# Kernel tuning notes

Hardware: AMD Instinct MI355X
Metric: run time of the kernel (lower is better)

Reference implementation:

```python
import jax, jax.numpy as jnp
import numpy as np

HS = 512   # hidden_size
IN = 2048  # input_size
MB = 100   # memory_bank_size
T  = 4096  # nImg


def setup_inputs() -> dict:
    key = jax.random.key(0)
    ks = jax.random.split(key, 20)

    def w(k, i, o):
        return jax.random.normal(k, (i, o), jnp.float32) * (1.0 / np.sqrt(i))

    def b(k, o):
        return jax.random.normal(k, (o,), jnp.float32) * 0.01

    return {
        "hidden_out_a": jax.random.normal(ks[0], (T, IN), jnp.float32),
        "hidden_out_m": jax.random.normal(ks[1], (T, IN), jnp.float32),
        "W_ca": w(ks[2], HS + IN, HS),  "b_ca": b(ks[3], HS),    # hidden_to_content_a
        "W_cm": w(ks[4], HS + IN, HS),  "b_cm": b(ks[5], HS),    # hidden_to_content_m
        "W_wp": w(ks[6], 3 * HS, 3),    "b_wp": b(ks[7], 3),     # write_prob
        "W_wpa": w(ks[8], HS + IN, MB), "b_wpa": b(ks[9], MB),   # write_prob_a
        "W_wpm": w(ks[10], HS + IN, MB),"b_wpm": b(ks[11], MB),  # write_prob_m
        "W_rp": w(ks[12], 3 * HS, MB),  "b_rp": b(ks[13], MB),   # read_prob
        "W_rh": w(ks[14], 2 * HS, HS),  "b_rh": b(ks[15], HS),   # read_to_hidden
        "W_rha": w(ks[16], 2 * HS + IN, HS), "b_rha": b(ks[17], HS),  # read_to_hidden_a
        "W_rhm": w(ks[18], 2 * HS + IN, HS), "b_rhm": b(ks[19], HS),  # read_to_hidden_m
        "nImg": T,
    }


def reference(hidden_out_a, hidden_out_m,
              W_ca, b_ca, W_cm, b_cm,
              W_wp, b_wp, W_wpa, b_wpa, W_wpm, b_wpm,
              W_rp, b_rp, W_rh, b_rh,
              W_rha, b_rha, W_rhm, b_rhm,
              nImg):
    hs = W_rh.shape[1]
    mb = W_rp.shape[1]

    def step(carry, xs):
        mem, h, ha, hm = carry            # mem: [MB, HS]; h/ha/hm: [HS]
        xa, xm = xs                       # [IN] each
        xh = jnp.concatenate([ha, hm, h])               # [3*HS]
        ar = jax.nn.softmax(xh @ W_rp + b_rp)           # [MB]
        r = ar @ mem                                    # [HS] memory read
        h1 = jax.nn.relu(jnp.concatenate([r, h]) @ W_rh + b_rh)
        ha1 = jax.nn.relu(jnp.concatenate([xa, r, ha]) @ W_rha + b_rha)
        hm1 = jax.nn.relu(jnp.concatenate([xm, r, hm]) @ W_rhm + b_rhm)
        aw = jax.nn.softmax(xh @ W_wp + b_wp)           # [3] stream gate
        xha = jnp.concatenate([ha, xa])                 # [HS+IN]
        xhm = jnp.concatenate([hm, xm])
        c_a = jax.nn.relu(xha @ W_ca + b_ca)            # [HS]
        c_m = jax.nn.relu(xhm @ W_cm + b_cm)
        aw_a = jax.nn.softmax(xha @ W_wpa + b_wpa)      # [MB]
        aw_m = jax.nn.softmax(xhm @ W_wpm + b_wpm)
        mem = aw[0] * mem + aw[1] * aw_a[:, None] * c_a + aw[2] * aw_m[:, None] * c_m
        return (mem, h1, ha1, hm1), h1

    init = (jnp.zeros((mb, hs), hidden_out_a.dtype),
            jnp.zeros((hs,), hidden_out_a.dtype),
            jnp.zeros((hs,), hidden_out_a.dtype),
            jnp.zeros((hs,), hidden_out_a.dtype))
    _, hiddens = jax.lax.scan(step, init,
                              (hidden_out_a[:nImg], hidden_out_m[:nImg]))
    return hiddens  # [nImg, HS]
```

## Files before the change

### kernel.cpp

```cpp
#include <hip/hip_runtime.h>
#include <cstdint>
#include <cstddef>

#define HS 512

constexpr int TPB  = 512;
constexpr int GBLK = 64;
constexpr int OWNB = 24;
constexpr int WPAD = 516;

constexpr size_t OFF_TWrp  = 0;
constexpr size_t OFF_TWwp  = OFF_TWrp  + 100*1536;
constexpr size_t OFF_TWwpa = OFF_TWwp  + 3*1536;
constexpr size_t OFF_TWwpm = OFF_TWwpa + 100*512;
constexpr size_t OFF_TWca  = OFF_TWwpm + 100*512;
constexpr size_t OFF_TWcm  = OFF_TWca  + 512*512;
constexpr size_t OFF_TWh0  = OFF_TWcm  + 512*512;
constexpr size_t OFF_TWh1  = OFF_TWh0  + 512*512;
constexpr size_t OFF_TWh2  = OFF_TWh1  + 512*512;
constexpr size_t OFF_TWu0  = OFF_TWh2  + 512*512;
constexpr size_t OFF_TWu1  = OFF_TWu0  + 512*512;
constexpr size_t OFF_TWu2  = OFF_TWu1  + 512*512;
constexpr size_t OFF_PAca  = OFF_TWu2  + 512*512;
constexpr size_t OFF_PMcm  = OFF_PAca  + 4096*512;
constexpr size_t OFF_PArha = OFF_PMcm  + 4096*512;
constexpr size_t OFF_PMrhm = OFF_PArha + 4096*512;
constexpr size_t OFF_PAwpa = OFF_PMrhm + 4096*512;
constexpr size_t OFF_PMwpm = OFF_PAwpa + 4096*100;
constexpr size_t OFF_CARRY = OFF_PMwpm + 4096*100;
constexpr size_t OFF_BCAST = OFF_CARRY + 2*1536*2;

__device__ __forceinline__ unsigned long long ald(const unsigned long long* p) {
  return __hip_atomic_load(const_cast<unsigned long long*>(p),
                           __ATOMIC_RELAXED, __HIP_MEMORY_SCOPE_AGENT);
}
__device__ __forceinline__ void gstTag(unsigned long long* p, float v, unsigned tag) {
  unsigned long long u = ((unsigned long long)tag << 32) | (unsigned long long)__float_as_uint(v);
  __hip_atomic_store(p, u, __ATOMIC_RELAXED, __HIP_MEMORY_SCOPE_AGENT);
}
__device__ __forceinline__ float xrsum(float v) {
  #pragma unroll
  for (int o = 32; o; o >>= 1) v += __shfl_xor(v, o, 64);
  return v;
}
__device__ __forceinline__ float rsum16(float v) {
  #pragma unroll
  for (int o = 8; o; o >>= 1) v += __shfl_xor(v, o, 64);
  return v;
}

template<int K4>
__device__ __forceinline__ float dotK(const float* __restrict__ w, const float* x) {
  int l = threadIdx.x & 63;
  const float4* w4 = (const float4*)w;
  const float4* x4 = (const float4*)x;
  float acc = 0.f;
  #pragma unroll
  for (int it = 0; it < K4; ++it) {
    float4 a = w4[l + 64*it];
    float4 b = x4[l + 64*it];
    acc += a.x*b.x + a.y*b.y + a.z*b.z + a.w*b.w;
  }
  return acc;
}

__device__ __forceinline__ float dot16_512(const float* __restrict__ w,
                                           const float* x, int gl) {
  const float4* w4 = (const float4*)w;
  const float4* x4 = (const float4*)x;
  float acc = 0.f;
  #pragma unroll
  for (int it = 0; it < 8; ++it) {
    float4 a = w4[gl + 16*it];
    float4 b = x4[gl + 16*it];
    acc += a.x*b.x + a.y*b.y + a.z*b.z + a.w*b.w;
  }
  return acc;
}

__device__ __forceinline__ void dot16_2x512(const float* __restrict__ w,
                                            const float* xa, const float* xm,
                                            int gl, float& ra, float& rm) {
  const float4* w4 = (const float4*)w;
  const float4* a4 = (const float4*)xa;
  const float4* m4 = (const float4*)xm;
  float sa = 0.f, sm = 0.f;
  #pragma unroll
  for (int it = 0; it < 8; ++it) {
    float4 wv = w4[gl + 16*it], av = a4[gl + 16*it], mv = m4[gl + 16*it];
    sa += wv.x*av.x + wv.y*av.y + wv.z*av.z + wv.w*av.w;
    sm += wv.x*mv.x + wv.y*mv.y + wv.z*mv.z + wv.w*mv.w;
  }
  #pragma unroll
  for (int o = 8; o; o >>= 1) { sa += __shfl_xor(sa, o, 64); sm += __shfl_xor(sm, o, 64); }
  ra = sa; rm = sm;
}

__global__ void initK(unsigned long long* carryT, unsigned long long* bcast) {
  int i = blockIdx.x * blockDim.x + threadIdx.x, st = gridDim.x * blockDim.x;
  for (int k = i; k < 1536; k += st) carryT[k] = (1ull << 32);
  for (int k = i; k < 1536; k += st) carryT[1536 + k] = 0ull;
  for (int k = i; k < 2 * 1344; k += st) bcast[k] = 0ull;
}

__global__ void transK(const float* __restrict__ src, float* __restrict__ dst, int R, int C) {
  __shared__ float tile[32][33];
  int c0 = blockIdx.x * 32, r0 = blockIdx.y * 32;
  for (int i = threadIdx.y; i < 32; i += 8) {
    int r = r0 + i, c = c0 + threadIdx.x;
    tile[i][threadIdx.x] = (r < R && c < C) ? src[(size_t)r * C + c] : 0.f;
  }
  __syncthreads();
  for (int i = threadIdx.y; i < 32; i += 8) {
    int c = c0 + i, r = r0 + threadIdx.x;
    if (c < C && r < R) dst[(size_t)c * R + r] = tile[threadIdx.x][i];
  }
}

__global__ __launch_bounds__(256) void gemmK(const float* __restrict__ X,
                                             const float* __restrict__ W,
                                             float* __restrict__ C, int N) {
  __shared__ float As[16][68];
  __shared__ float Bs[16][68];
  int t0 = blockIdx.y * 64, n0 = blockIdx.x * 64;
  int tid = threadIdx.x, tx = tid & 15, ty = tid >> 4;
  float acc[4][4] = {};
  for (int k0 = 0; k0 < 2048; k0 += 16) {
    {
      int r = tid >> 2, c = (tid & 3) * 4;
      float4 v = *(const float4*)(X + (size_t)(t0 + r) * 2048 + k0 + c);
      As[c + 0][r] = v.x; As[c + 1][r] = v.y; As[c + 2][r] = v.z; As[c + 3][r] = v.w;
    }
    {
      int kr = tid >> 4, c = (tid & 15) * 4;
      int gcol = n0 + c;
      const float* src = W + (size_t)(k0 + kr) * N + gcol;
      #pragma unroll
      for (int i = 0; i < 4; ++i) Bs[kr][c + i] = (gcol + i < N) ? src[i] : 0.f;
    }
    __syncthreads();
    #pragma unroll
    for (int kk = 0; kk < 16; ++kk) {
      float4 a4 = *(const float4*)&As[kk][ty * 4];
      float4 b4 = *(const float4*)&Bs[kk][tx * 4];
      float av[4] = {a4.x, a4.y, a4.z, a4.w};
      float bv[4] = {b4.x, b4.y, b4.z, b4.w};
      #pragma unroll
      for (int i = 0; i < 4; ++i)
        #pragma unroll
        for (int j = 0; j < 4; ++j) acc[i][j] += av[i] * bv[j];
    }
    __syncthreads();
  }
  #pragma unroll
  for (int i = 0; i < 4; ++i)
    #pragma unroll
    for (int j = 0; j < 4; ++j) {
      int col = n0 + tx * 4 + j;
      if (col < N) C[(size_t)(t0 + ty * 4 + i) * N + col] = acc[i][j];
    }
}

__global__ __launch_bounds__(256) void gemm128(const float* __restrict__ X,
                                               const float* __restrict__ W,
                                               float* __restrict__ C) {
  __shared__ float As[8][132];
  __shared__ float Bs[8][132];
  const int N = 512;
  int t0 = blockIdx.y * 128, n0 = blockIdx.x * 128;
  int tid = threadIdx.x, tx = tid & 15, ty = tid >> 4;
  float acc[8][8] = {};
  for (int k0 = 0; k0 < 2048; k0 += 8) {
    int r = tid >> 1, c4 = (tid & 1) * 4;
    float4 va = *(const float4*)(X + (size_t)(t0 + r) * 2048 + k0 + c4);
    int kr = tid >> 5, cb = (tid & 31) * 4;
    float4 vb = *(const float4*)(W + (size_t)(k0 + kr) * N + n0 + cb);
    __syncthreads();
    As[c4 + 0][r] = va.x; As[c4 + 1][r] = va.y; As[c4 + 2][r] = va.z; As[c4 + 3][r] = va.w;
    Bs[kr][cb] = vb.x; Bs[kr][cb + 1] = vb.y; Bs[kr][cb + 2] = vb.z; Bs[kr][cb + 3] = vb.w;
    __syncthreads();
    #pragma unroll
    for (int kk = 0; kk < 8; ++kk) {
      float av[8], bv[8];
      *(float4*)av       = *(const float4*)&As[kk][ty * 8];
      *(float4*)(av + 4) = *(const float4*)&As[kk][ty * 8 + 4];
      *(float4*)bv       = *(const float4*)&Bs[kk][tx * 8];
      *(float4*)(bv + 4) = *(const float4*)&Bs[kk][tx * 8 + 4];
      #pragma unroll
      for (int i = 0; i < 8; ++i)
        #pragma unroll
        for (int j = 0; j < 8; ++j) acc[i][j] += av[i] * bv[j];
    }
  }
  #pragma unroll
  for (int i = 0; i < 8; ++i) {
    float* dst = C + (size_t)(t0 + ty * 8 + i) * N + n0 + tx * 8;
    *(float4*)dst       = *(float4*)&acc[i][0];
    *(float4*)(dst + 4) = *(float4*)&acc[i][4];
  }
}

struct RArgs {
  const float *TWrp, *TWwp, *TWwpa, *TWwpm, *TWca, *TWcm;
  const float *TWh0, *TWh1, *TWh2, *TWu0, *TWu1, *TWu2;
  const float *PAca, *PMcm, *PArha, *PMrhm, *PAwpa, *PMwpm;
  const float *b_ca, *b_cm, *b_wp, *b_wpa, *b_wpm, *b_rp, *b_rh, *b_rha, *b_rhm;
  unsigned long long *carryT, *bcast;
  float *out;
  int nT;
};

__global__ __launch_bounds__(TPB, 1) void recurK(RArgs a) {
  const int tid  = threadIdx.x;
  const int lane = tid & 63;
  const int lw   = tid >> 6;
  const int g    = tid >> 4;
  const int gl   = tid & 15;
  const int b    = blockIdx.x;

  __shared__ __align__(16) float s_wca[8 * WPAD];
  __shared__ __align__(16) float s_wcm[8 * WPAD];
  __shared__ __align__(16) float s_wbig[2 * 1536];
  __shared__ __align__(16) float s_wsm[4 * WPAD];
  __shared__ __align__(16) float s_TWu[OWNB * WPAD];
  __shared__ __align__(16) float s_G[OWNB * 112];
  __shared__ __align__(16) float s_x[1536];
  __shared__ __align__(16) float s_c[1024];
  __shared__ float s_ar[112], s_awa[112], s_awm[112], s_aw[4];

  const int r0a = (b + 51) & 63;
  const int r1m = (b + 25) & 63;
  const bool big1_grp = (b < 36);
  const bool big1_wp  = (b >= 40 && b <= 42);

  for (int i = tid; i < 8 * WPAD; i += TPB) {
    int row = i / WPAD, col = i - row * WPAD;
    if (col < 512) {
      s_wca[i] = a.TWca[(size_t)(b * 8 + row) * 512 + col];
      s_wcm[i] = a.TWcm[(size_t)(b * 8 + row) * 512 + col];
    }
  }
  for (int i = tid; i < 1536; i += TPB) {
    s_wbig[i] = a.TWrp[(size_t)b * 1536 + i];
    float v2 = 0.f;
    if (big1_grp)      v2 = a.TWrp[(size_t)(b + 64) * 1536 + i];
    else if (big1_wp)  v2 = a.TWwp[(size_t)(b - 40) * 1536 + i];
    s_wbig[1536 + i] = v2;
  }
  for (int i = tid; i < 4 * WPAD; i += TPB) {
    int sl = i / WPAD, col = i - sl * WPAD;
    float v = 0.f;
    if (col < 512) {
      if (sl == 0)      v = a.TWwpa[(size_t)r0a * 512 + col];
      else if (sl == 1) v = (r0a < 36) ? a.TWwpa[(size_t)(r0a + 64) * 512 + col] : 0.f;
      else if (sl == 2) v = a.TWwpm[(size_t)r1m * 512 + col];
      else              v = (r1m < 36) ? a.TWwpm[(size_t)(r1m + 64) * 512 + col] : 0.f;
    }
    s_wsm[i] = v;
  }
  for (int i = tid; i < OWNB * WPAD; i += TPB) {
    int rr = i / WPAD, col = i - rr * WPAD;
    if (col < 512) {
      int q = b * OWNB + rr, hsel = q >> 9, j = q & 511;
      const float* src = (hsel == 0) ? a.TWu0 : (hsel == 1) ? a.TWu1 : a.TWu2;
      s_TWu[i] = src[(size_t)j * 512 + col];
    }
  }
  for (int i = tid; i < OWNB * 112; i += TPB) s_G[i] = 0.f;
  if (tid < 112) { s_ar[tid] = 0.f; s_awa[tid] = 0.f; s_awm[tid] = 0.f; }

  int dstA = -1, xoffA = 0, strideA = 512, rowA = 0;
  float biasA = 0.f;
  const float* preAPtr = nullptr;
  if (lw < 2) {
    int col = b * 8 + g; rowA = g;
    dstA = col; biasA = a.b_ca[col]; preAPtr = a.PAca + col;
  } else if (lw < 4) {
    int col = b * 8 + (g - 8); rowA = g - 8;
    dstA = 512 + col; biasA = a.b_cm[col]; preAPtr = a.PMcm + col;
  } else if (lw == 4) {
    int sl = g - 16;
    if (sl == 0)                  { rowA = 0; dstA = 1124 + r0a;      biasA = a.b_wpa[r0a];      preAPtr = a.PAwpa + r0a;      xoffA = 0;   strideA = 100; }
    else if (sl == 1 && r0a < 36) { rowA = 1; dstA = 1124 + r0a + 64; biasA = a.b_wpa[r0a + 64]; preAPtr = a.PAwpa + r0a + 64; xoffA = 0;   strideA = 100; }
    else if (sl == 2)             { rowA = 2; dstA = 1224 + r1m;      biasA = a.b_wpm[r1m];      preAPtr = a.PMwpm + r1m;      xoffA = 512; strideA = 100; }
    else if (sl == 3 && r1m < 36) { rowA = 3; dstA = 1224 + r1m + 64; biasA = a.b_wpm[r1m + 64]; preAPtr = a.PMwpm + r1m + 64; xoffA = 512; strideA = 100; }
  }
  int dstBig = -1, bigOff = 0;
  float biasBig = 0.f;
  if (lw == 6) { dstBig = 1024 + b; biasBig = a.b_rp[b]; bigOff = 0; }
  else if (lw == 7) {
    if (big1_grp)      { dstBig = 1024 + b + 64;  biasBig = a.b_rp[b + 64]; bigOff = 1536; }
    else if (big1_wp)  { dstBig = 1324 + (b - 40); biasBig = a.b_wp[b - 40]; bigOff = 1536; }
  }
  int ownHsel = 0, ownJ = 0, whXo = 0;
  float biasO = 0.f;
  const float* preOPtr = nullptr;
  const float* whPtr = nullptr;
  if (g < OWNB) {
    int q = b * OWNB + g, hsel = q >> 9, j = q & 511;
    ownHsel = hsel; ownJ = j;
    if (hsel == 0)      { biasO = a.b_rh[j];                           whPtr = a.TWh0 + (size_t)j * 512; whXo = 1024; }
    else if (hsel == 1) { biasO = a.b_rha[j]; preOPtr = a.PArha + j;   whPtr = a.TWh1 + (size_t)j * 512; whXo = 0; }
    else                { biasO = a.b_rhm[j]; preOPtr = a.PMrhm + j;   whPtr = a.TWh2 + (size_t)j * 512; whXo = 512; }
  }
  __syncthreads();

  float whv = 0.f;
  for (int t = 0; t < a.nT; ++t) {
    const unsigned tagB = (unsigned)t + 1;
    unsigned long long* bc = a.bcast + (size_t)(t & 1) * 1344;

    float preA = preAPtr ? preAPtr[(size_t)t * strideA] : 0.f;
    float preO = preOPtr ? preOPtr[(size_t)t * 512] : 0.f;

    {
      const unsigned long long* cin = a.carryT + (size_t)(t & 1) * 1536;
      int i0 = tid, i1 = tid + 512, i2 = tid + 1024;
      unsigned long long v0 = ald(cin + i0), v1 = ald(cin + i1), v2 = ald(cin + i2);
      while (((unsigned)(v0 >> 32) < tagB) | ((unsigned)(v1 >> 32) < tagB) |
             ((unsigned)(v2 >> 32) < tagB)) {
        __builtin_amdgcn_s_sleep(1);
        v0 = ald(cin + i0); v1 = ald(cin + i1); v2 = ald(cin + i2);
      }
      s_x[i0] = __uint_as_float((unsigned)v0);
      s_x[i1] = __uint_as_float((unsigned)v1);
      s_x[i2] = __uint_as_float((unsigned)v2);
    }
    __syncthreads();

    if (lw < 2) {
      float v = rsum16(dot16_512(s_wca + rowA * WPAD, s_x, gl));
      if (!gl) gstTag(bc + dstA, fmaxf(v + preA + biasA, 0.f), tagB);
    } else if (lw < 4) {
      float v = rsum16(dot16_512(s_wcm + rowA * WPAD, s_x + 512, gl));
      if (!gl) gstTag(bc + dstA, fmaxf(v + preA + biasA, 0.f), tagB);
    } else if (lw == 4) {
      if (dstA >= 0) {
        float v = rsum16(dot16_512(s_wsm + rowA * WPAD, s_x + xoffA, gl));
        if (!gl) gstTag(bc + dstA, v + preA + biasA, tagB);
      }
    } else if (lw >= 6) {
      if (dstBig >= 0) {
        float v = xrsum(dotK<6>(s_wbig + bigOff, s_x));
        if (!lane) gstTag(bc + dstBig, v + biasBig, tagB);
      }
    }
    if (g < OWNB) whv = rsum16(dot16_512(whPtr, s_x + whXo, gl));

    if (lw < 3) {
      int base = 1024 + lw * 100;
      const unsigned long long* p1 = bc + base + lane;
      bool two = lane < 36;
      unsigned long long v1 = ald(p1);
      unsigned long long v2 = two ? ald(p1 + 64) : ~0ull;
      while (((unsigned)(v1 >> 32) < tagB) | ((unsigned)(v2 >> 32) < tagB)) {
        __builtin_amdgcn_s_sleep(1);
        v1 = ald(p1); if (two) v2 = ald(p1 + 64);
      }
      float x1 = __uint_as_float((unsigned)v1);
      float x2 = two ? __uint_as_float((unsigned)v2) : -3.0e38f;
      float m = fmaxf(x1, x2);
      #pragma unroll
      for (int o = 32; o; o >>= 1) m = fmaxf(m, __shfl_xor(m, o, 64));
      float e1 = expf(x1 - m);
      float e2 = two ? expf(x2 - m) : 0.f;
      float ss = e1 + e2;
      #pragma unroll
      for (int o = 32; o; o >>= 1) ss += __shfl_xor(ss, o, 64);
      float inv = 1.f / ss;
      float* dst = (lw == 0) ? s_ar : (lw == 1) ? s_awa : s_awm;
      dst[lane] = e1 * inv;
      if (two) dst[64 + lane] = e2 * inv;
    } else if (lw == 3) {
      float x = -3.0e38f;
      if (lane < 3) {
        const unsigned long long* p = bc + 1324 + lane;
        unsigned long long v = ald(p);
        while ((unsigned)(v >> 32) < tagB) { __builtin_amdgcn_s_sleep(1); v = ald(p); }
        x = __uint_as_float((unsigned)v);
      }
      float m = x;
      #pragma unroll
      for (int o = 32; o; o >>= 1) m = fmaxf(m, __shfl_xor(m, o, 64));
      float e = (lane < 3) ? expf(x - m) : 0.f;
      float ss = e;
      #pragma unroll
      for (int o = 32; o; o >>= 1) ss += __shfl_xor(ss, o, 64);
      if (lane < 3) s_aw[lane] = e / ss;
    } else {
      int base = tid - 256;
      const unsigned long long* p = bc + base;
      unsigned long long v0 = ald(p), v1 = ald(p + 256), v2 = ald(p + 512), v3 = ald(p + 768);
      while (((unsigned)(v0 >> 32) < tagB) | ((unsigned)(v1 >> 32) < tagB) |
             ((unsigned)(v2 >> 32) < tagB) | ((unsigned)(v3 >> 32) < tagB)) {
        __builtin_amdgcn_s_sleep(1);
        v0 = ald(p); v1 = ald(p + 256); v2 = ald(p + 512); v3 = ald(p + 768);
      }
      s_c[base]       = __uint_as_float((unsigned)v0);
      s_c[base + 256] = __uint_as_float((unsigned)v1);
      s_c[base + 512] = __uint_as_float((unsigned)v2);
      s_c[base + 768] = __uint_as_float((unsigned)v3);
    }
    __syncthreads();

    unsigned long long* cout = a.carryT + (size_t)((t + 1) & 1) * 1536;
    if (g < OWNB) {
      const float aw0 = s_aw[0], aw1 = s_aw[1], aw2 = s_aw[2];
      float uA, uM;
      dot16_2x512(s_TWu + g * WPAD, s_c, s_c + 512, gl, uA, uM);

      float* grow = s_G + g * 112;
      float gv[7];
      float contrib = 0.f;
      #pragma unroll
      for (int k = 0; k < 7; ++k) {
        int idx = gl + 16 * k;
        gv[k] = grow[idx];
        contrib += s_ar[idx] * gv[k];
      }
      contrib = rsum16(contrib);
      if (!gl) {
        float h = fmaxf(contrib + whv + preO + biasO, 0.f);
        if (ownHsel == 0) {
          a.out[(size_t)t * 512 + ownJ] = h;
          gstTag(cout + 1024 + ownJ, h, tagB + 1);
        } else if (ownHsel == 1) {
          gstTag(cout + ownJ, h, tagB + 1);
        } else {
          gstTag(cout + 512 + ownJ, h, tagB + 1);
        }
      }
      #pragma unroll
      for (int k = 0; k < 7; ++k) {
        int idx = gl + 16 * k;
        grow[idx] = aw0 * gv[k] + aw1 * s_awa[idx] * uA + aw2 * s_awm[idx] * uM;
      }
    }
  }
}

extern "C" void kernel_launch(void* const* d_in, const int* in_sizes, int n_in,
                              void* d_out, int out_size, void* d_ws, size_t ws_size,
                              hipStream_t stream) {
  const float* Xa    = (const float*)d_in[0];
  const float* Xm    = (const float*)d_in[1];
  const float* W_ca  = (const float*)d_in[2];  const float* b_ca  = (const float*)d_in[3];
  const float* W_cm  = (const float*)d_in[4];  const float* b_cm  = (const float*)d_in[5];
  const float* W_wp  = (const float*)d_in[6];  const float* b_wp  = (const float*)d_in[7];
  const float* W_wpa = (const float*)d_in[8];  const float* b_wpa = (const float*)d_in[9];
  const float* W_wpm = (const float*)d_in[10]; const float* b_wpm = (const float*)d_in[11];
  const float* W_rp  = (const float*)d_in[12]; const float* b_rp  = (const float*)d_in[13];
  const float* W_rh  = (const float*)d_in[14]; const float* b_rh  = (const float*)d_in[15];
  const float* W_rha = (const float*)d_in[16]; const float* b_rha = (const float*)d_in[17];
  const float* W_rhm = (const float*)d_in[18]; const float* b_rhm = (const float*)d_in[19];

  int nT = out_size / HS;
  float* ws = (float*)d_ws;

  initK<<<dim3(64), dim3(256), 0, stream>>>(
      (unsigned long long*)(ws + OFF_CARRY),
      (unsigned long long*)(ws + OFF_BCAST));

  dim3 tb(32, 8);
  auto tg = [](int R, int C) { return dim3((C + 31) / 32, (R + 31) / 32); };
  transK<<<tg(1536, 100), tb, 0, stream>>>(W_rp,                       ws + OFF_TWrp,  1536, 100);
  transK<<<tg(1536, 3),   tb, 0, stream>>>(W_wp,                       ws + OFF_TWwp,  1536, 3);
  transK<<<tg(512, 100),  tb, 0, stream>>>(W_wpa,                      ws + OFF_TWwpa, 512, 100);
  transK<<<tg(512, 100),  tb, 0, stream>>>(W_wpm,                      ws + OFF_TWwpm, 512, 100);
  transK<<<tg(512, 512),  tb, 0, stream>>>(W_ca,                       ws + OFF_TWca,  512, 512);
  transK<<<tg(512, 512),  tb, 0, stream>>>(W_cm,                       ws + OFF_TWcm,  512, 512);
  transK<<<tg(512, 512),  tb, 0, stream>>>(W_rh  + 512 * 512,          ws + OFF_TWh0,  512, 512);
  transK<<<tg(512, 512),  tb, 0, stream>>>(W_rha + (size_t)2560 * 512, ws + OFF_TWh1,  512, 512);
  transK<<<tg(512, 512),  tb, 0, stream>>>(W_rhm + (size_t)2560 * 512, ws + OFF_TWh2,  512, 512);
  transK<<<tg(512, 512),  tb, 0, stream>>>(W_rh,                       ws + OFF_TWu0,  512, 512);
  transK<<<tg(512, 512),  tb, 0, stream>>>(W_rha + (size_t)2048 * 512, ws + OFF_TWu1,  512, 512);
  transK<<<tg(512, 512),  tb, 0, stream>>>(W_rhm + (size_t)2048 * 512, ws + OFF_TWu2,  512, 512);

  int tB = nT / 128;
  gemm128<<<dim3(4, tB), dim3(256), 0, stream>>>(Xa, W_ca + (size_t)512 * 512, ws + OFF_PAca);
  gemm128<<<dim3(4, tB), dim3(256), 0, stream>>>(Xm, W_cm + (size_t)512 * 512, ws + OFF_PMcm);
  gemm128<<<dim3(4, tB), dim3(256), 0, stream>>>(Xa, W_rha,                    ws + OFF_PArha);
  gemm128<<<dim3(4, tB), dim3(256), 0, stream>>>(Xm, W_rhm,                    ws + OFF_PMrhm);
  int tB64 = nT / 64;
  gemmK<<<dim3(2, tB64), dim3(256), 0, stream>>>(Xa, W_wpa + (size_t)512 * 100, ws + OFF_PAwpa, 100);
  gemmK<<<dim3(2, tB64), dim3(256), 0, stream>>>(Xm, W_wpm + (size_t)512 * 100, ws + OFF_PMwpm, 100);

  RArgs a;
  a.TWrp  = ws + OFF_TWrp;  a.TWwp  = ws + OFF_TWwp;
  a.TWwpa = ws + OFF_TWwpa; a.TWwpm = ws + OFF_TWwpm;
  a.TWca  = ws + OFF_TWca;  a.TWcm  = ws + OFF_TWcm;
  a.TWh0  = ws + OFF_TWh0;  a.TWh1  = ws + OFF_TWh1;  a.TWh2 = ws + OFF_TWh2;
  a.TWu0  = ws + OFF_TWu0;  a.TWu1  = ws + OFF_TWu1;  a.TWu2 = ws + OFF_TWu2;
  a.PAca  = ws + OFF_PAca;  a.PMcm  = ws + OFF_PMcm;
  a.PArha = ws + OFF_PArha; a.PMrhm = ws + OFF_PMrhm;
  a.PAwpa = ws + OFF_PAwpa; a.PMwpm = ws + OFF_PMwpm;
  a.b_ca = b_ca; a.b_cm = b_cm; a.b_wp = b_wp; a.b_wpa = b_wpa; a.b_wpm = b_wpm;
  a.b_rp = b_rp; a.b_rh = b_rh; a.b_rha = b_rha; a.b_rhm = b_rhm;
  a.carryT = (unsigned long long*)(ws + OFF_CARRY);
  a.bcast  = (unsigned long long*)(ws + OFF_BCAST);
  a.out    = (float*)d_out;
  a.nT     = nT;

  recurK<<<dim3(GBLK), dim3(TPB), 0, stream>>>(a);
}
```

Before: 25.18 ms.

## Replace per-element tagged payloads with per-block tag flags plus plain float payloads

Cross-block communication in the persistent recurrent kernel previously packed a tag with every 64-bit element and spun on each element. It now writes plain float payloads, drains memory with a waitcnt and a block barrier, then publishes one tag per block. Consumers in one wavefront poll all 64 block tags before bulk-loading the payloads. This halves payload traffic and removes per-element polling, in exchange for an extra block barrier per phase; the payload layout is also reorganised into per-block 24-float slots, and the shared-memory row pad changes.

Result: slower. 27.27 ms (+8.3%).

```diff
diff --git a/kernel.cpp b/kernel.cpp
--- a/kernel.cpp
+++ b/kernel.cpp
@@ -7,7 +7,7 @@
 constexpr int TPB  = 512;
 constexpr int GBLK = 64;
 constexpr int OWNB = 24;
-constexpr int WPAD = 516;
+constexpr int WPAD = 520;
 
 constexpr size_t OFF_TWrp  = 0;
 constexpr size_t OFF_TWwp  = OFF_TWrp  + 100*1536;
@@ -27,16 +27,24 @@
 constexpr size_t OFF_PMrhm = OFF_PArha + 4096*512;
 constexpr size_t OFF_PAwpa = OFF_PMrhm + 4096*512;
 constexpr size_t OFF_PMwpm = OFF_PAwpa + 4096*100;
-constexpr size_t OFF_CARRY = OFF_PMwpm + 4096*100;
-constexpr size_t OFF_BCAST = OFF_CARRY + 2*1536*2;
+constexpr size_t OFF_CPAY  = OFF_PMwpm + 4096*100;
+constexpr size_t OFF_CTAG  = OFF_CPAY  + 2*1536;
+constexpr size_t OFF_BPAY  = OFF_CTAG  + 2*64;
+constexpr size_t OFF_BTAG  = OFF_BPAY  + 2*1536;
 
 __device__ __forceinline__ unsigned long long ald(const unsigned long long* p) {
   return __hip_atomic_load(const_cast<unsigned long long*>(p),
                            __ATOMIC_RELAXED, __HIP_MEMORY_SCOPE_AGENT);
 }
-__device__ __forceinline__ void gstTag(unsigned long long* p, float v, unsigned tag) {
-  unsigned long long u = ((unsigned long long)tag << 32) | (unsigned long long)__float_as_uint(v);
-  __hip_atomic_store(p, u, __ATOMIC_RELAXED, __HIP_MEMORY_SCOPE_AGENT);
+__device__ __forceinline__ float aldf(const float* p) {
+  return __hip_atomic_load(const_cast<float*>(p),
+                           __ATOMIC_RELAXED, __HIP_MEMORY_SCOPE_AGENT);
+}
+__device__ __forceinline__ void astf(float* p, float v) {
+  __hip_atomic_store(p, v, __ATOMIC_RELAXED, __HIP_MEMORY_SCOPE_AGENT);
+}
+__device__ __forceinline__ void astu(unsigned* p, unsigned v) {
+  __hip_atomic_store(p, v, __ATOMIC_RELAXED, __HIP_MEMORY_SCOPE_AGENT);
 }
 __device__ __forceinline__ float xrsum(float v) {
   #pragma unroll
@@ -96,11 +104,14 @@
   ra = sa; rm = sm;
 }
 
-__global__ void initK(unsigned long long* carryT, unsigned long long* bcast) {
+__global__ void initK(float* cpay, unsigned* ctag, float* bpay, unsigned* btag) {
   int i = blockIdx.x * blockDim.x + threadIdx.x, st = gridDim.x * blockDim.x;
-  for (int k = i; k < 1536; k += st) carryT[k] = (1ull << 32);
-  for (int k = i; k < 1536; k += st) carryT[1536 + k] = 0ull;
-  for (int k = i; k < 2 * 1344; k += st) bcast[k] = 0ull;
+  for (int k = i; k < 2 * 1536; k += st) cpay[k] = 0.f;
+  for (int k = i; k < 2 * 1536; k += st) bpay[k] = 0.f;
+  for (int k = i; k < 64; k += st) {
+    ctag[k] = 1u;  ctag[64 + k] = 0u;
+    btag[k] = 0u;  btag[64 + k] = 0u;
+  }
 }
 
 __global__ void transK(const float* __restrict__ src, float* __restrict__ dst, int R, int C) {
@@ -205,7 +216,8 @@
   const float *TWh0, *TWh1, *TWh2, *TWu0, *TWu1, *TWu2;
   const float *PAca, *PMcm, *PArha, *PMrhm, *PAwpa, *PMwpm;
   const float *b_ca, *b_cm, *b_wp, *b_wpa, *b_wpm, *b_rp, *b_rh, *b_rha, *b_rhm;
-  unsigned long long *carryT, *bcast;
+  float *cpay, *bpay;
+  unsigned *ctag, *btag;
   float *out;
   int nT;
 };
@@ -269,96 +281,126 @@
   for (int i = tid; i < OWNB * 112; i += TPB) s_G[i] = 0.f;
   if (tid < 112) { s_ar[tid] = 0.f; s_awa[tid] = 0.f; s_awm[tid] = 0.f; }
 
-  int dstA = -1, xoffA = 0, strideA = 512, rowA = 0;
+  int pslA = -1, xoffA = 0, strideA = 512, rowA = 0;
+  bool reluA = false;
   float biasA = 0.f;
   const float* preAPtr = nullptr;
+  const float* wA = nullptr;
   if (lw < 2) {
     int col = b * 8 + g; rowA = g;
-    dstA = col; biasA = a.b_ca[col]; preAPtr = a.PAca + col;
+    pslA = g; reluA = true; biasA = a.b_ca[col]; preAPtr = a.PAca + col;
+    wA = s_wca; xoffA = 0;
   } else if (lw < 4) {
     int col = b * 8 + (g - 8); rowA = g - 8;
-    dstA = 512 + col; biasA = a.b_cm[col]; preAPtr = a.PMcm + col;
+    pslA = 8 + (g - 8); reluA = true; biasA = a.b_cm[col]; preAPtr = a.PMcm + col;
+    wA = s_wcm; xoffA = 512;
   } else if (lw == 4) {
     int sl = g - 16;
-    if (sl == 0)                  { rowA = 0; dstA = 1124 + r0a;      biasA = a.b_wpa[r0a];      preAPtr = a.PAwpa + r0a;      xoffA = 0;   strideA = 100; }
-    else if (sl == 1 && r0a < 36) { rowA = 1; dstA = 1124 + r0a + 64; biasA = a.b_wpa[r0a + 64]; preAPtr = a.PAwpa + r0a + 64; xoffA = 0;   strideA = 100; }
-    else if (sl == 2)             { rowA = 2; dstA = 1224 + r1m;      biasA = a.b_wpm[r1m];      preAPtr = a.PMwpm + r1m;      xoffA = 512; strideA = 100; }
-    else if (sl == 3 && r1m < 36) { rowA = 3; dstA = 1224 + r1m + 64; biasA = a.b_wpm[r1m + 64]; preAPtr = a.PMwpm + r1m + 64; xoffA = 512; strideA = 100; }
-  }
-  int dstBig = -1, bigOff = 0;
+    wA = s_wsm; strideA = 100;
+    if (sl == 0)                  { rowA = 0; pslA = 18; biasA = a.b_wpa[r0a];      preAPtr = a.PAwpa + r0a;      xoffA = 0;   }
+    else if (sl == 1 && r0a < 36) { rowA = 1; pslA = 19; biasA = a.b_wpa[r0a + 64]; preAPtr = a.PAwpa + r0a + 64; xoffA = 0;   }
+    else if (sl == 2)             { rowA = 2; pslA = 20; biasA = a.b_wpm[r1m];      preAPtr = a.PMwpm + r1m;      xoffA = 512; }
+    else if (sl == 3 && r1m < 36) { rowA = 3; pslA = 21; biasA = a.b_wpm[r1m + 64]; preAPtr = a.PMwpm + r1m + 64; xoffA = 512; }
+    else pslA = -1;
+  }
+  int pslBig = -1, bigOff = 0;
   float biasBig = 0.f;
-  if (lw == 6) { dstBig = 1024 + b; biasBig = a.b_rp[b]; bigOff = 0; }
+  if (lw == 6) { pslBig = 16; biasBig = a.b_rp[b]; bigOff = 0; }
   else if (lw == 7) {
-    if (big1_grp)      { dstBig = 1024 + b + 64;  biasBig = a.b_rp[b + 64]; bigOff = 1536; }
-    else if (big1_wp)  { dstBig = 1324 + (b - 40); biasBig = a.b_wp[b - 40]; bigOff = 1536; }
-  }
-  int ownHsel = 0, ownJ = 0, whXo = 0;
+    if (big1_grp)      { pslBig = 17; biasBig = a.b_rp[b + 64]; bigOff = 1536; }
+    else if (big1_wp)  { pslBig = 17; biasBig = a.b_wp[b - 40]; bigOff = 1536; }
+  }
+  const int rr = g - 8;
+  const bool own = (g >= 8);
+  int ownHsel = 0, ownJ = 0, whXo = 0, qOwn = 0;
   float biasO = 0.f;
   const float* preOPtr = nullptr;
   const float* whPtr = nullptr;
-  if (g < OWNB) {
-    int q = b * OWNB + g, hsel = q >> 9, j = q & 511;
+  if (own) {
+    qOwn = b * OWNB + rr;
+    int hsel = qOwn >> 9, j = qOwn & 511;
     ownHsel = hsel; ownJ = j;
     if (hsel == 0)      { biasO = a.b_rh[j];                           whPtr = a.TWh0 + (size_t)j * 512; whXo = 1024; }
     else if (hsel == 1) { biasO = a.b_rha[j]; preOPtr = a.PArha + j;   whPtr = a.TWh1 + (size_t)j * 512; whXo = 0; }
     else                { biasO = a.b_rhm[j]; preOPtr = a.PMrhm + j;   whPtr = a.TWh2 + (size_t)j * 512; whXo = 512; }
   }
+  auto xidx = [](int q) { int hs = q >> 9, j = q & 511;
+                          return (hs == 0 ? 1024 : hs == 1 ? 0 : 512) + j; };
+  const int xi0 = xidx(tid), xi1 = xidx(tid + 512), xi2 = xidx(tid + 1024);
+  const int p0 = tid - 256;
   __syncthreads();
 
   float whv = 0.f;
   for (int t = 0; t < a.nT; ++t) {
     const unsigned tagB = (unsigned)t + 1;
-    unsigned long long* bc = a.bcast + (size_t)(t & 1) * 1344;
+    const int par = t & 1;
 
     float preA = preAPtr ? preAPtr[(size_t)t * strideA] : 0.f;
     float preO = preOPtr ? preOPtr[(size_t)t * 512] : 0.f;
 
+    if (lw == 0) {
+      const unsigned long long* tp =
+          (const unsigned long long*)(a.ctag + (size_t)par * 64);
+      int ok;
+      do {
+        ok = 1;
+        if (lane < 32) {
+          unsigned long long v = ald(tp + lane);
+          ok = ((unsigned)v >= tagB) && ((unsigned)(v >> 32) >= tagB);
+        }
+      } while (!__all(ok));
+    }
+    __syncthreads();
+
     {
-      const unsigned long long* cin = a.carryT + (size_t)(t & 1) * 1536;
-      int i0 = tid, i1 = tid + 512, i2 = tid + 1024;
-      unsigned long long v0 = ald(cin + i0), v1 = ald(cin + i1), v2 = ald(cin + i2);
-      while (((unsigned)(v0 >> 32) < tagB) | ((unsigned)(v1 >> 32) < tagB) |
-             ((unsigned)(v2 >> 32) < tagB)) {
-        __builtin_amdgcn_s_sleep(1);
-        v0 = ald(cin + i0); v1 = ald(cin + i1); v2 = ald(cin + i2);
-      }
-      s_x[i0] = __uint_as_float((unsigned)v0);
-      s_x[i1] = __uint_as_float((unsigned)v1);
-      s_x[i2] = __uint_as_float((unsigned)v2);
-    }
-    __syncthreads();
-
-    if (lw < 2) {
-      float v = rsum16(dot16_512(s_wca + rowA * WPAD, s_x, gl));
-      if (!gl) gstTag(bc + dstA, fmaxf(v + preA + biasA, 0.f), tagB);
-    } else if (lw < 4) {
-      float v = rsum16(dot16_512(s_wcm + rowA * WPAD, s_x + 512, gl));
-      if (!gl) gstTag(bc + dstA, fmaxf(v + preA + biasA, 0.f), tagB);
-    } else if (lw == 4) {
-      if (dstA >= 0) {
-        float v = rsum16(dot16_512(s_wsm + rowA * WPAD, s_x + xoffA, gl));
-        if (!gl) gstTag(bc + dstA, v + preA + biasA, tagB);
+      const float* cp = a.cpay + (size_t)par * 1536;
+      float v0 = aldf(cp + tid), v1 = aldf(cp + tid + 512), v2 = aldf(cp + tid + 1024);
+      s_x[xi0] = v0; s_x[xi1] = v1; s_x[xi2] = v2;
+    }
+    __syncthreads();
+
+    float* bpo = a.bpay + (size_t)par * 1536;
+    if (lw < 5) {
+      if (pslA >= 0) {
+        float v = rsum16(dot16_512(wA + rowA * WPAD, s_x + xoffA, gl));
+        if (!gl) {
+          v += preA + biasA;
+          if (reluA) v = fmaxf(v, 0.f);
+          astf(bpo + b * 24 + pslA, v);
+        }
       }
     } else if (lw >= 6) {
-      if (dstBig >= 0) {
+      if (pslBig >= 0) {
         float v = xrsum(dotK<6>(s_wbig + bigOff, s_x));
-        if (!lane) gstTag(bc + dstBig, v + biasBig, tagB);
+        if (!lane) astf(bpo + b * 24 + pslBig, v + biasBig);
       }
     }
-    if (g < OWNB) whv = rsum16(dot16_512(whPtr, s_x + whXo, gl));
-
-    if (lw < 3) {
-      int base = 1024 + lw * 100;
-      const unsigned long long* p1 = bc + base + lane;
+    asm volatile("s_waitcnt vmcnt(0)" ::: "memory");
+    __syncthreads();
+    if (tid == 0) astu(a.btag + (size_t)par * 64 + b, tagB);
+
+    if (own) whv = rsum16(dot16_512(whPtr, s_x + whXo, gl));
+
+    if (lw == 0) {
+      const unsigned long long* tp =
+          (const unsigned long long*)(a.btag + (size_t)par * 64);
+      int ok;
+      do {
+        ok = 1;
+        if (lane < 32) {
+          unsigned long long v = ald(tp + lane);
+          ok = ((unsigned)v >= tagB) && ((unsigned)(v >> 32) >= tagB);
+        }
+      } while (!__all(ok));
+    }
+    __syncthreads();
+
+    const float* bp = a.bpay + (size_t)par * 1536;
+    if (lw == 0) {
+      unsigned long long v = ald((const unsigned long long*)(bp + lane * 24 + 16));
       bool two = lane < 36;
-      unsigned long long v1 = ald(p1);
-      unsigned long long v2 = two ? ald(p1 + 64) : ~0ull;
-      while (((unsigned)(v1 >> 32) < tagB) | ((unsigned)(v2 >> 32) < tagB)) {
-        __builtin_amdgcn_s_sleep(1);
-        v1 = ald(p1); if (two) v2 = ald(p1 + 64);
-      }
-      float x1 = __uint_as_float((unsigned)v1);
-      float x2 = two ? __uint_as_float((unsigned)v2) : -3.0e38f;
+      float x1 = __uint_as_float((unsigned)v);
+      float x2 = two ? __uint_as_float((unsigned)(v >> 32)) : -3.0e38f;
       float m = fmaxf(x1, x2);
       #pragma unroll
       for (int o = 32; o; o >>= 1) m = fmaxf(m, __shfl_xor(m, o, 64));
@@ -368,17 +410,45 @@
       #pragma unroll
       for (int o = 32; o; o >>= 1) ss += __shfl_xor(ss, o, 64);
       float inv = 1.f / ss;
-      float* dst = (lw == 0) ? s_ar : (lw == 1) ? s_awa : s_awm;
-      dst[lane] = e1 * inv;
-      if (two) dst[64 + lane] = e2 * inv;
+      s_ar[lane] = e1 * inv;
+      if (two) s_ar[64 + lane] = e2 * inv;
+    } else if (lw == 1) {
+      unsigned long long v =
+          ald((const unsigned long long*)(bp + ((lane + 13) & 63) * 24 + 18));
+      bool two = lane < 36;
+      float x1 = __uint_as_float((unsigned)v);
+      float x2 = two ? __uint_as_float((unsigned)(v >> 32)) : -3.0e38f;
+      float m = fmaxf(x1, x2);
+      #pragma unroll
+      for (int o = 32; o; o >>= 1) m = fmaxf(m, __shfl_xor(m, o, 64));
+      float e1 = expf(x1 - m);
+      float e2 = two ? expf(x2 - m) : 0.f;
+      float ss = e1 + e2;
+      #pragma unroll
+      for (int o = 32; o; o >>= 1) ss += __shfl_xor(ss, o, 64);
+      float inv = 1.f / ss;
+      s_awa[lane] = e1 * inv;
+      if (two) s_awa[64 + lane] = e2 * inv;
+    } else if (lw == 2) {
+      unsigned long long v =
+          ald((const unsigned long long*)(bp + ((lane + 39) & 63) * 24 + 20));
+      bool two = lane < 36;
+      float x1 = __uint_as_float((unsigned)v);
+      float x2 = two ? __uint_as_float((unsigned)(v >> 32)) : -3.0e38f;
+      float m = fmaxf(x1, x2);
+      #pragma unroll
+      for (int o = 32; o; o >>= 1) m = fmaxf(m, __shfl_xor(m, o, 64));
+      float e1 = expf(x1 - m);
+      float e2 = two ? expf(x2 - m) : 0.f;
+      float ss = e1 + e2;
+      #pragma unroll
+      for (int o = 32; o; o >>= 1) ss += __shfl_xor(ss, o, 64);
+      float inv = 1.f / ss;
+      s_awm[lane] = e1 * inv;
+      if (two) s_awm[64 + lane] = e2 * inv;
     } else if (lw == 3) {
       float x = -3.0e38f;
-      if (lane < 3) {
-        const unsigned long long* p = bc + 1324 + lane;
-        unsigned long long v = ald(p);
-        while ((unsigned)(v >> 32) < tagB) { __builtin_amdgcn_s_sleep(1); v = ald(p); }
-        x = __uint_as_float((unsigned)v);
-      }
+      if (lane < 3) x = aldf(bp + (40 + lane) * 24 + 17);
       float m = x;
       #pragma unroll
       for (int o = 32; o; o >>= 1) m = fmaxf(m, __shfl_xor(m, o, 64));
@@ -388,29 +458,24 @@
       for (int o = 32; o; o >>= 1) ss += __shfl_xor(ss, o, 64);
       if (lane < 3) s_aw[lane] = e / ss;
     } else {
-      int base = tid - 256;
-      const unsigned long long* p = bc + base;
-      unsigned long long v0 = ald(p), v1 = ald(p + 256), v2 = ald(p + 512), v3 = ald(p + 768);
-      while (((unsigned)(v0 >> 32) < tagB) | ((unsigned)(v1 >> 32) < tagB) |
-             ((unsigned)(v2 >> 32) < tagB) | ((unsigned)(v3 >> 32) < tagB)) {
-        __builtin_amdgcn_s_sleep(1);
-        v0 = ald(p); v1 = ald(p + 256); v2 = ald(p + 512); v3 = ald(p + 768);
-      }
-      s_c[base]       = __uint_as_float((unsigned)v0);
-      s_c[base + 256] = __uint_as_float((unsigned)v1);
-      s_c[base + 512] = __uint_as_float((unsigned)v2);
-      s_c[base + 768] = __uint_as_float((unsigned)v3);
-    }
-    __syncthreads();
-
-    unsigned long long* cout = a.carryT + (size_t)((t + 1) & 1) * 1536;
-    if (g < OWNB) {
-      const float aw0 = s_aw[0], aw1 = s_aw[1], aw2 = s_aw[2];
-      float uA, uM;
-      dot16_2x512(s_TWu + g * WPAD, s_c, s_c + 512, gl, uA, uM);
-
-      float* grow = s_G + g * 112;
-      float gv[7];
+      unsigned long long va =
+          ald((const unsigned long long*)(bp + (p0 >> 2) * 24 + 2 * (p0 & 3)));
+      unsigned long long vm =
+          ald((const unsigned long long*)(bp + (p0 >> 2) * 24 + 8 + 2 * (p0 & 3)));
+      *(float2*)&s_c[2 * p0] =
+          make_float2(__uint_as_float((unsigned)va), __uint_as_float((unsigned)(va >> 32)));
+      *(float2*)&s_c[512 + 2 * p0] =
+          make_float2(__uint_as_float((unsigned)vm), __uint_as_float((unsigned)(vm >> 32)));
+    }
+    __syncthreads();
+
+    float* cpo = a.cpay + (size_t)((t + 1) & 1) * 1536;
+    float aw0 = 0.f, aw1 = 0.f, aw2 = 0.f, uA = 0.f, uM = 0.f;
+    float gv[7];
+    if (own) {
+      aw0 = s_aw[0]; aw1 = s_aw[1]; aw2 = s_aw[2];
+      dot16_2x512(s_TWu + (size_t)rr * WPAD, s_c, s_c + 512, gl, uA, uM);
+      float* grow = s_G + rr * 112;
       float contrib = 0.f;
       #pragma unroll
       for (int k = 0; k < 7; ++k) {
@@ -421,15 +486,16 @@
       contrib = rsum16(contrib);
       if (!gl) {
         float h = fmaxf(contrib + whv + preO + biasO, 0.f);
-        if (ownHsel == 0) {
-          a.out[(size_t)t * 512 + ownJ] = h;
-          gstTag(cout + 1024 + ownJ, h, tagB + 1);
-        } else if (ownHsel == 1) {
-          gstTag(cout + ownJ, h, tagB + 1);
-        } else {
-          gstTag(cout + 512 + ownJ, h, tagB + 1);
-        }
+        if (ownHsel == 0) a.out[(size_t)t * 512 + ownJ] = h;
+        astf(cpo + qOwn, h);
       }
+    }
+    asm volatile("s_waitcnt vmcnt(0)" ::: "memory");
+    __syncthreads();
+    if (tid == 0) astu(a.ctag + (size_t)((t + 1) & 1) * 64 + b, tagB + 1);
+
+    if (own) {
+      float* grow = s_G + rr * 112;
       #pragma unroll
       for (int k = 0; k < 7; ++k) {
         int idx = gl + 16 * k;
@@ -458,8 +524,8 @@
   float* ws = (float*)d_ws;
 
   initK<<<dim3(64), dim3(256), 0, stream>>>(
-      (unsigned long long*)(ws + OFF_CARRY),
-      (unsigned long long*)(ws + OFF_BCAST));
+      ws + OFF_CPAY, (unsigned*)(ws + OFF_CTAG),
+      ws + OFF_BPAY, (unsigned*)(ws + OFF_BTAG));
 
   dim3 tb(32, 8);
   auto tg = [](int R, int C) { return dim3((C + 31) / 32, (R + 31) / 32); };
@@ -496,8 +562,8 @@
   a.PAwpa = ws + OFF_PAwpa; a.PMwpm = ws + OFF_PMwpm;
   a.b_ca = b_ca; a.b_cm = b_cm; a.b_wp = b_wp; a.b_wpa = b_wpa; a.b_wpm = b_wpm;
   a.b_rp = b_rp; a.b_rh = b_rh; a.b_rha = b_rha; a.b_rhm = b_rhm;
-  a.carryT = (unsigned long long*)(ws + OFF_CARRY);
-  a.bcast  = (unsigned long long*)(ws + OFF_BCAST);
+  a.cpay = ws + OFF_CPAY;  a.ctag = (unsigned*)(ws + OFF_CTAG);
+  a.bpay = ws + OFF_BPAY;  a.btag = (unsigned*)(ws + OFF_BTAG);
   a.out    = (float*)d_out;
   a.nT     = nT;
 
```
